# Kernel optimization log

Hardware: AMD Instinct MI355X
Metric: run time of the kernel (lower is better)

The kernel has to match this reference:

```python
import jax, jax.numpy as jnp
import numpy as np

B, T, F, G, H, N, C = 32, 64, 32, 32, 256, 20000, 32
EPS = 1e-5


def setup_inputs() -> dict:
    key = jax.random.key(0)
    ks = jax.random.split(key, 24)
    s = 0.05
    d = {}
    d["data_feats"] = jax.random.normal(ks[0], (B, T, F), jnp.float32)
    d["gat_output"] = jax.random.normal(ks[1], (B, N, G), jnp.float32)
    d["row_ids"] = jax.random.randint(ks[2], (B, T), 0, 2 * N, jnp.int32)
    d["node_ids"] = jax.random.randint(ks[3], (N,), 0, 2 * N, jnp.int32)
    # shared LSTM (2 layers): layer0 input F+G, layer1 input H; b = b_ih + b_hh fused
    d["shared_Wih0"] = jax.random.normal(ks[4], (4 * H, F + G)) * s
    d["shared_Whh0"] = jax.random.normal(ks[5], (4 * H, H)) * s
    d["shared_b0"] = jax.random.normal(ks[6], (4 * H,)) * s
    d["shared_Wih1"] = jax.random.normal(ks[7], (4 * H, H)) * s
    d["shared_Whh1"] = jax.random.normal(ks[8], (4 * H, H)) * s
    d["shared_b1"] = jax.random.normal(ks[9], (4 * H,)) * s
    # act/time/timeR LSTMs stacked on leading axis 3, each 2 layers of [4H,H]
    d["heads_Wih"] = jax.random.normal(ks[10], (3, 2, 4 * H, H)) * s
    d["heads_Whh"] = jax.random.normal(ks[11], (3, 2, 4 * H, H)) * s
    d["heads_b"] = jax.random.normal(ks[12], (3, 2, 4 * H)) * s
    d["bn_gnn_g"] = jnp.ones((G,), jnp.float32)
    d["bn_gnn_b"] = jnp.zeros((G,), jnp.float32)
    d["bn_shared_g"] = jnp.ones((H,), jnp.float32)
    d["bn_shared_b"] = jnp.zeros((H,), jnp.float32)
    d["heads_bn_g"] = jnp.ones((3, H), jnp.float32)
    d["heads_bn_b"] = jnp.zeros((3, H), jnp.float32)
    d["fc_act_W"] = jax.random.normal(ks[13], (C, H)) * s
    d["fc_act_b"] = jnp.zeros((C,), jnp.float32)
    d["fc_time_W"] = jax.random.normal(ks[14], (1, H)) * s
    d["fc_time_b"] = jnp.zeros((1,), jnp.float32)
    d["fc_timeR_W"] = jax.random.normal(ks[15], (1, H)) * s
    d["fc_timeR_b"] = jnp.zeros((1,), jnp.float32)
    return d


def batchnorm(x, gamma, beta):
    # BatchNorm1d training-mode: stats over (batch, length) per channel; x: [B, L, C]
    mean = jnp.mean(x, axis=(0, 1))
    var = jnp.var(x, axis=(0, 1))
    return (x - mean) * (gamma / jnp.sqrt(var + EPS)) + beta


def lstm_layer(x, Wih, Whh, b):
    # x: [B, T, Din]; PyTorch gate order i, f, g, o
    xp = jnp.einsum("btf,gf->btg", x, Wih) + b  # [B, T, 4H]
    h = Whh.shape[1]
    init = (jnp.zeros((x.shape[0], h), x.dtype), jnp.zeros((x.shape[0], h), x.dtype))

    def step(carry, xt):
        hprev, cprev = carry
        gates = xt + hprev @ Whh.T
        i, f, g, o = jnp.split(gates, 4, axis=-1)
        c = jax.nn.sigmoid(f) * cprev + jax.nn.sigmoid(i) * jnp.tanh(g)
        hnew = jax.nn.sigmoid(o) * jnp.tanh(c)
        return (hnew, c), hnew

    _, hs = jax.lax.scan(step, init, jnp.swapaxes(xp, 0, 1))
    return jnp.swapaxes(hs, 0, 1)  # [B, T, H]


def reference(data_feats, gat_output, row_ids, node_ids,
              shared_Wih0, shared_Whh0, shared_b0,
              shared_Wih1, shared_Whh1, shared_b1,
              heads_Wih, heads_Whh, heads_b,
              bn_gnn_g, bn_gnn_b, bn_shared_g, bn_shared_b,
              heads_bn_g, heads_bn_b,
              fc_act_W, fc_act_b, fc_time_W, fc_time_b, fc_timeR_W, fc_timeR_b):
    # --- graph branch: BN over GAT output, value-match lookup + gather ---
    gat_norm = batchnorm(gat_output, bn_gnn_g, bn_gnn_b)  # [B, N, G]
    eq = row_ids[:, :, None] == node_ids[None, None, :]   # [B, T, N]
    idx = jnp.argmax(eq, axis=-1)                          # first matching index
    found = jnp.any(eq, axis=-1)
    gathered = jnp.take_along_axis(gat_norm, idx[:, :, None], axis=1)  # [B, T, G]
    matched = jnp.where(found[:, :, None], gathered, 0.0)
    lstm_in = jnp.concatenate([data_feats, matched], axis=-1)  # [B, T, F+G]

    # --- shared 2-layer LSTM + BN (dropout off / eval) ---
    shared = lstm_layer(lstm_in, shared_Wih0, shared_Whh0, shared_b0)
    shared = lstm_layer(shared, shared_Wih1, shared_Whh1, shared_b1)
    shared = batchnorm(shared, bn_shared_g, bn_shared_b)

    # --- act / time / timeR head LSTMs (vmapped over the 3 heads) + BN ---
    def head(Wih, Whh, b, g, bb):
        hh = lstm_layer(shared, Wih[0], Whh[0], b[0])
        hh = lstm_layer(hh, Wih[1], Whh[1], b[1])
        return batchnorm(hh, g, bb)

    heads = jax.vmap(head)(heads_Wih, heads_Whh, heads_b, heads_bn_g, heads_bn_b)
    last = heads[:, :, -1, :]  # [3, B, H]

    act = jax.nn.softmax(last[0] @ fc_act_W.T + fc_act_b, axis=1)
    time = last[1] @ fc_time_W.T + fc_time_b
    timeR = last[2] @ fc_timeR_W.T + fc_timeR_b
    return act, time, timeR
```

## Files before the change

### kernel.cpp

```cpp
#include <hip/hip_runtime.h>
#include <hip/hip_fp16.h>
#include <math.h>

#define Bn 32
#define Tn 64
#define Fdim 32
#define Gdim 32
#define Hdim 256
#define Ndim 20000
#define Cdim 32
#define G4 1024
#define BT 2048
#define EPSc 1e-5f

__device__ __forceinline__ float sigmoidf_(float x){ return 1.0f/(1.0f + __expf(-x)); }
__device__ __forceinline__ float tanhf_(float x){ return 2.0f/(1.0f+__expf(-2.0f*x)) - 1.0f; }

typedef _Float16 h2t __attribute__((ext_vector_type(2)));

__device__ __forceinline__ float fdot2_(unsigned w, unsigned h, float acc){
#if defined(__has_builtin) && __has_builtin(__builtin_amdgcn_fdot2)
  return __builtin_amdgcn_fdot2(__builtin_bit_cast(h2t, w), __builtin_bit_cast(h2t, h), acc, false);
#else
  h2t a = __builtin_bit_cast(h2t, w), b = __builtin_bit_cast(h2t, h);
  acc = fmaf((float)a.x, (float)b.x, acc);
  return fmaf((float)a.y, (float)b.y, acc);
#endif
}

__device__ __forceinline__ unsigned packh_(float lo, float hi){
  unsigned ulo = (unsigned)__half_as_ushort(__float2half(lo));
  unsigned uhi = (unsigned)__half_as_ushort(__float2half(hi));
  return ulo | (uhi << 16);
}

__global__ void init_kernel(float* ws){
  int i = blockIdx.x*256 + threadIdx.x;
  if (i < 2112) ws[i] = 0.0f;
  int* table = (int*)(ws + 2112);
  if (i < 40000) table[i] = 0x7fffffff;
}

__global__ void bn_stats_kernel(const float* __restrict__ gat, float* __restrict__ sums){
  __shared__ float ss[256], sq[256];
  int tid = threadIdx.x;
  int idx = blockIdx.x*256 + tid;
  int stride = gridDim.x*256;
  const int total = Bn*Ndim*Gdim;
  float s=0.f,q=0.f;
  for (int i=idx; i<total; i+=stride){ float v = gat[i]; s+=v; q+=v*v; }
  ss[tid]=s; sq[tid]=q; __syncthreads();
  for (int off=128; off>=32; off>>=1){
    if(tid<off){ ss[tid]+=ss[tid+off]; sq[tid]+=sq[tid+off]; }
    __syncthreads();
  }
  if (tid<32){ atomicAdd(&sums[tid], ss[tid]); atomicAdd(&sums[32+tid], sq[tid]); }
}

__global__ void table_kernel(const int* __restrict__ node_ids, int* __restrict__ table){
  int i = blockIdx.x*256 + threadIdx.x;
  if (i < Ndim) atomicMin(&table[node_ids[i]], i);
}

__global__ void build_input_kernel(const float* __restrict__ feats, const float* __restrict__ gat,
    const int* __restrict__ row_ids, const int* __restrict__ table, const float* __restrict__ sums,
    const float* __restrict__ bng, const float* __restrict__ bnb, unsigned* __restrict__ out){
  int gt = blockIdx.x*256 + threadIdx.x;
  int pos = gt >> 5; int k2 = gt & 31;
  float lo, hi;
  if (k2 < 16){
    float2 v = *(const float2*)(feats + pos*Fdim + 2*k2);
    lo = v.x; hi = v.y;
  } else {
    int g0 = 2*(k2-16);
    int r = row_ids[pos];
    int idx = table[r];
    if (idx < Ndim){
      int b = pos / Tn;
      float2 x = *(const float2*)(gat + (size_t)(b*Ndim + idx)*Gdim + g0);
      const float cnt = (float)(Bn*Ndim);
      float m0 = sums[g0]/cnt,   v0 = sums[32+g0]/cnt - m0*m0;
      float m1 = sums[g0+1]/cnt, v1 = sums[32+g0+1]/cnt - m1*m1;
      lo = (x.x-m0)*bng[g0]*rsqrtf(v0+EPSc) + bnb[g0];
      hi = (x.y-m1)*bng[g0+1]*rsqrtf(v1+EPSc) + bnb[g0+1];
    } else { lo = 0.0f; hi = 0.0f; }
  }
  out[gt] = packh_(lo, hi);
}

struct TArgs { const float* src[8]; unsigned* dst[8]; int K[8]; };
__global__ void packwih_kernel(TArgs a){
  __shared__ unsigned tile[32][33];
  int mat = blockIdx.y;
  int K = a.K[mat];
  int K2 = K >> 1;
  int ktiles = K2 >> 5;
  int tk = blockIdx.x & 3;
  int tn = blockIdx.x >> 2;
  if (tk >= ktiles) return;
  const float* src = a.src[mat];
  unsigned* dst = a.dst[mat];
  int tx = threadIdx.x, ty = threadIdx.y;
  int n0 = tn*32, k2_0 = tk*32;
  #pragma unroll
  for (int i=0;i<4;i++){
    int nn = ty + 8*i;
    const float* p = src + (size_t)(n0+nn)*K + 2*(k2_0 + tx);
    tile[nn][tx] = packh_(p[0], p[1]);
  }
  __syncthreads();
  #pragma unroll
  for (int i=0;i<4;i++){
    int r = ty + 8*i;
    dst[(size_t)(k2_0 + r)*G4 + n0 + tx] = tile[tx][r];
  }
}

struct PkArgs { const float* src[8]; };
__global__ void pack_kernel(PkArgs a, unsigned* __restrict__ dst){
  int gid = blockIdx.x*256 + threadIdx.x;
  int m = gid >> 17;
  int rem = gid & 0x1FFFF;
  int q = rem & 3;
  int t2 = (rem >> 2) & 1023;
  int ci = rem >> 12;
  int c = ci >> 3, i = ci & 7;
  int j = t2 & 255, kq = t2 >> 8;
  int r = 4*j + c;
  int k = kq*64 + 8*i + 2*q;
  const float* W = a.src[m];
  dst[gid] = packh_(W[r*256 + k], W[r*256 + k + 1]);
}

struct PArgs { const unsigned* x[3]; const unsigned* wt[3]; const float* bias[3]; float* out[3]; int K2; };
__global__ __launch_bounds__(256) void proj_kernel(PArgs a){
  int hd = blockIdx.z;
  int n  = blockIdx.y*256 + threadIdx.x;
  int m0 = blockIdx.x*8;
  int K2 = a.K2;
  const unsigned* xh = a.x[hd] + (size_t)m0*K2;
  const unsigned* wt = a.wt[hd];
  float bv = a.bias[hd][n];
  float acc[8];
  #pragma unroll
  for (int i=0;i<8;i++) acc[i]=bv;
  for (int k2=0;k2<K2;k2+=4){
    unsigned w0 = wt[(size_t)(k2+0)*G4+n];
    unsigned w1 = wt[(size_t)(k2+1)*G4+n];
    unsigned w2 = wt[(size_t)(k2+2)*G4+n];
    unsigned w3 = wt[(size_t)(k2+3)*G4+n];
    #pragma unroll
    for (int i=0;i<8;i++){
      uint4 xv = *(const uint4*)(xh + i*K2 + k2);
      acc[i]=fdot2_(w0,xv.x,acc[i]); acc[i]=fdot2_(w1,xv.y,acc[i]);
      acc[i]=fdot2_(w2,xv.z,acc[i]); acc[i]=fdot2_(w3,xv.w,acc[i]);
    }
  }
  float* out = a.out[hd] + (size_t)m0*G4 + n;
  #pragma unroll
  for (int i=0;i<8;i++) out[i*G4]=acc[i];
}

struct RArgs { const float* xp[3]; const unsigned* wt[3]; float* out[3]; unsigned* outh[3]; };
__global__ __launch_bounds__(1024,1) void rec_kernel(RArgs a){
  extern __shared__ float lds[];
  unsigned* lw   = (unsigned*)lds;
  float*    part = lds + 32768;
  unsigned* hp   = (unsigned*)(lds + 36864);
  int b = blockIdx.x, hd = blockIdx.y, tid = threadIdx.x;
  int j = tid & 255, kq = tid >> 8;
  const float* xp = a.xp[hd] + (size_t)b*Tn*G4;
  const unsigned* wt = a.wt[hd];
  float* out = a.out[hd] + (size_t)b*Tn*Hdim;
  unsigned* outh = a.outh[hd] + (size_t)b*Tn*128;

  unsigned w[96];
  #pragma unroll
  for (int c=0;c<4;c++){
    #pragma unroll
    for (int i=0;i<6;i++){
      uint4 v = *(const uint4*)(wt + ((c*8+i)*1024 + tid)*4);
      w[(c*6+i)*4+0]=v.x; w[(c*6+i)*4+1]=v.y; w[(c*6+i)*4+2]=v.z; w[(c*6+i)*4+3]=v.w;
    }
    #pragma unroll
    for (int i=6;i<8;i++){
      uint4 v = *(const uint4*)(wt + ((c*8+i)*1024 + tid)*4);
      *(uint4*)(lw + ((c*2+(i-6))*1024 + tid)*4) = v;
    }
  }
  float cst = 0.0f;
  if (tid < 128){ hp[tid] = 0u; hp[128+tid] = 0u; }
  __syncthreads();

  int p = 0;
  for (int t=0; t<Tn; t++){
    float ac0, ac1, ac2, ac3;
    if (kq == 0){
      float4 xv = *(const float4*)(xp + t*G4 + 4*j);
      ac0=xv.x; ac1=xv.y; ac2=xv.z; ac3=xv.w;
    } else { ac0=0.f; ac1=0.f; ac2=0.f; ac3=0.f; }
    const unsigned* hrow = hp + p*128 + kq*32;
    #pragma unroll
    for (int ic=0; ic<6; ic++){
      uint4 hv = *(const uint4*)(hrow + 4*ic);
      ac0=fdot2_(w[0*24+ic*4+0],hv.x,ac0); ac0=fdot2_(w[0*24+ic*4+1],hv.y,ac0);
      ac0=fdot2_(w[0*24+ic*4+2],hv.z,ac0); ac0=fdot2_(w[0*24+ic*4+3],hv.w,ac0);
      ac1=fdot2_(w[1*24+ic*4+0],hv.x,ac1); ac1=fdot2_(w[1*24+ic*4+1],hv.y,ac1);
      ac1=fdot2_(w[1*24+ic*4+2],hv.z,ac1); ac1=fdot2_(w[1*24+ic*4+3],hv.w,ac1);
      ac2=fdot2_(w[2*24+ic*4+0],hv.x,ac2); ac2=fdot2_(w[2*24+ic*4+1],hv.y,ac2);
      ac2=fdot2_(w[2*24+ic*4+2],hv.z,ac2); ac2=fdot2_(w[2*24+ic*4+3],hv.w,ac2);
      ac3=fdot2_(w[3*24+ic*4+0],hv.x,ac3); ac3=fdot2_(w[3*24+ic*4+1],hv.y,ac3);
      ac3=fdot2_(w[3*24+ic*4+2],hv.z,ac3); ac3=fdot2_(w[3*24+ic*4+3],hv.w,ac3);
    }
    #pragma unroll
    for (int ic=6; ic<8; ic++){
      uint4 hv = *(const uint4*)(hrow + 4*ic);
      { uint4 lv = *(const uint4*)(lw + ((0*2+(ic-6))*1024 + tid)*4);
        ac0=fdot2_(lv.x,hv.x,ac0); ac0=fdot2_(lv.y,hv.y,ac0);
        ac0=fdot2_(lv.z,hv.z,ac0); ac0=fdot2_(lv.w,hv.w,ac0); }
      { uint4 lv = *(const uint4*)(lw + ((1*2+(ic-6))*1024 + tid)*4);
        ac1=fdot2_(lv.x,hv.x,ac1); ac1=fdot2_(lv.y,hv.y,ac1);
        ac1=fdot2_(lv.z,hv.z,ac1); ac1=fdot2_(lv.w,hv.w,ac1); }
      { uint4 lv = *(const uint4*)(lw + ((2*2+(ic-6))*1024 + tid)*4);
        ac2=fdot2_(lv.x,hv.x,ac2); ac2=fdot2_(lv.y,hv.y,ac2);
        ac2=fdot2_(lv.z,hv.z,ac2); ac2=fdot2_(lv.w,hv.w,ac2); }
      { uint4 lv = *(const uint4*)(lw + ((3*2+(ic-6))*1024 + tid)*4);
        ac3=fdot2_(lv.x,hv.x,ac3); ac3=fdot2_(lv.y,hv.y,ac3);
        ac3=fdot2_(lv.z,hv.z,ac3); ac3=fdot2_(lv.w,hv.w,ac3); }
    }
    *(float4*)(part + kq*1024 + 4*j) = make_float4(ac0,ac1,ac2,ac3);
    __syncthreads();
    if (tid < 256){
      int u = tid;
      float gi = part[u]     + part[1024+u]     + part[2048+u]     + part[3072+u];
      float gf = part[256+u] + part[1024+256+u] + part[2048+256+u] + part[3072+256+u];
      float gg = part[512+u] + part[1024+512+u] + part[2048+512+u] + part[3072+512+u];
      float go = part[768+u] + part[1024+768+u] + part[2048+768+u] + part[3072+768+u];
      cst = sigmoidf_(gf)*cst + sigmoidf_(gi)*tanhf_(gg);
      float h = sigmoidf_(go)*tanhf_(cst);
      out[t*Hdim + u] = h;
      float hpartner = __shfl_xor(h, 1);
      if ((u & 1) == 0){
        unsigned hh = packh_(h, hpartner);
        hp[(p^1)*128 + (u>>1)] = hh;
        outh[t*128 + (u>>1)] = hh;
      }
    }
    __syncthreads();
    p ^= 1;
  }
}

struct SArgs { const float* in[3]; float* stats[3]; };
__global__ void stats_kernel(SArgs a){
  int hd = blockIdx.y; int tid = threadIdx.x;
  const float* in = a.in[hd] + blockIdx.x*256*Hdim;
  float s=0.f,q=0.f;
  for (int r=0;r<256;r++){ float v = in[r*Hdim + tid]; s+=v; q+=v*v; }
  atomicAdd(&a.stats[hd][tid], s);
  atomicAdd(&a.stats[hd][Hdim+tid], q);
}

__global__ void norm_kernel(const float* __restrict__ in, const float* __restrict__ stats,
   const float* __restrict__ g, const float* __restrict__ bta, unsigned* __restrict__ outh){
  int i2 = blockIdx.x*256 + threadIdx.x;
  int h2 = i2 & 127; int m = i2 >> 7;
  int h0 = 2*h2;
  float2 v = *(const float2*)(in + (size_t)m*Hdim + h0);
  float m0 = stats[h0]*(1.0f/BT),   v0 = stats[Hdim+h0]*(1.0f/BT) - m0*m0;
  float m1 = stats[h0+1]*(1.0f/BT), v1 = stats[Hdim+h0+1]*(1.0f/BT) - m1*m1;
  float lo = (v.x-m0)*g[h0]*rsqrtf(v0+EPSc) + bta[h0];
  float hi = (v.y-m1)*g[h0+1]*rsqrtf(v1+EPSc) + bta[h0+1];
  outh[i2] = packh_(lo, hi);
}

__global__ __launch_bounds__(256) void final_kernel(
  const float* __restrict__ h0, const float* __restrict__ h1, const float* __restrict__ h2,
  const float* __restrict__ stats,
  const float* __restrict__ hbg, const float* __restrict__ hbb,
  const float* __restrict__ actW, const float* __restrict__ actB,
  const float* __restrict__ tW, const float* __restrict__ tB,
  const float* __restrict__ rW, const float* __restrict__ rB,
  float* __restrict__ outp){
  __shared__ float v0[Bn*Hdim];
  __shared__ float lg[Bn*Cdim];
  int tid = threadIdx.x;
  for (int i=tid; i<Bn*Hdim; i+=256){
    int b=i>>8, h=i&255;
    float sm = stats[512 + h], sq = stats[512+256+h];
    float mean = sm*(1.0f/BT); float var = sq*(1.0f/BT) - mean*mean;
    v0[i] = (h0[(b*Tn+63)*Hdim + h] - mean)*hbg[h]*rsqrtf(var+EPSc) + hbb[h];
  }
  __syncthreads();
  for (int i=tid; i<Bn*Cdim; i+=256){
    int b=i>>5, cc=i&31;
    float acc = actB[cc];
    const float* wrow = actW + cc*Hdim;
    const float* vrow = v0 + b*Hdim;
    #pragma unroll 4
    for (int h=0;h<Hdim;h++) acc = fmaf(vrow[h], wrow[h], acc);
    lg[i] = acc;
  }
  __syncthreads();
  if (tid < Bn){
    int b = tid;
    float m = -1e30f;
    #pragma unroll
    for (int cc=0; cc<Cdim; cc++) m = fmaxf(m, lg[b*Cdim+cc]);
    float e[Cdim]; float s = 0.f;
    #pragma unroll
    for (int cc=0; cc<Cdim; cc++){ float ee = __expf(lg[b*Cdim+cc]-m); e[cc]=ee; s+=ee; }
    float inv = 1.0f/s;
    #pragma unroll
    for (int cc=0; cc<Cdim; cc++) outp[b*Cdim+cc] = e[cc]*inv;
  }
  if (tid < 64){
    int b = tid & 31; int w = tid >> 5;
    const float* hh = w ? h2 : h1;
    const float* fw = w ? rW : tW;
    float fb = w ? rB[0] : tB[0];
    int hd = 1 + w;
    float acc = fb;
    for (int h=0; h<Hdim; h++){
      float sm = stats[(1+hd)*512 + h], sq = stats[(1+hd)*512+256+h];
      float mean = sm*(1.0f/BT); float var = sq*(1.0f/BT) - mean*mean;
      float v = (hh[(b*Tn+63)*Hdim + h] - mean)*hbg[hd*Hdim+h]*rsqrtf(var+EPSc) + hbb[hd*Hdim+h];
      acc = fmaf(v, fw[h], acc);
    }
    outp[1024 + w*32 + b] = acc;
  }
}

extern "C" void kernel_launch(void* const* d_in, const int* in_sizes, int n_in,
                              void* d_out, int out_size, void* d_ws, size_t ws_size,
                              hipStream_t stream){
  const float* data_feats = (const float*)d_in[0];
  const float* gat   = (const float*)d_in[1];
  const int*   row_ids  = (const int*)d_in[2];
  const int*   node_ids = (const int*)d_in[3];
  const float* sWih0 = (const float*)d_in[4];
  const float* sWhh0 = (const float*)d_in[5];
  const float* sb0   = (const float*)d_in[6];
  const float* sWih1 = (const float*)d_in[7];
  const float* sWhh1 = (const float*)d_in[8];
  const float* sb1   = (const float*)d_in[9];
  const float* hWih  = (const float*)d_in[10];
  const float* hWhh  = (const float*)d_in[11];
  const float* hb    = (const float*)d_in[12];
  const float* bng   = (const float*)d_in[13];
  const float* bnb   = (const float*)d_in[14];
  const float* bsg   = (const float*)d_in[15];
  const float* bsb   = (const float*)d_in[16];
  const float* hbg   = (const float*)d_in[17];
  const float* hbb   = (const float*)d_in[18];
  const float* actW  = (const float*)d_in[19];
  const float* actB  = (const float*)d_in[20];
  const float* tW    = (const float*)d_in[21];
  const float* tB    = (const float*)d_in[22];
  const float* rW    = (const float*)d_in[23];
  const float* rB    = (const float*)d_in[24];
  float* ws  = (float*)d_ws;
  float* out = (float*)d_out;

  const size_t S_GAT = 0;
  const size_t S_BN  = 64;
  const size_t TABLE = 2112;
  const size_t WIHP  = 42112;
  const size_t PSLOT = 131072;
  const size_t WHHP  = WIHP + 8*PSLOT;
  const size_t LSTM_INH = WHHP + 8*PSLOT;
  const size_t XPOFF = LSTM_INH + 65536;
  const size_t BUF0H = XPOFF + 3*2097152;
  const size_t BUF1  = BUF0H + 262144;
  const size_t BUFNH = BUF1 + 524288;
  const size_t HB0H  = BUFNH + 262144;
  const size_t HB1   = HB0H + 3*262144;

  const int REC_LDS = 148480;
  hipFuncSetAttribute((const void*)rec_kernel, hipFuncAttributeMaxDynamicSharedMemorySize, REC_LDS);

  init_kernel<<<157,256,0,stream>>>(ws);
  bn_stats_kernel<<<2048,256,0,stream>>>(gat, ws+S_GAT);
  table_kernel<<<(Ndim+255)/256,256,0,stream>>>(node_ids, (int*)(ws+TABLE));
  build_input_kernel<<<256,256,0,stream>>>(data_feats, gat, row_ids, (int*)(ws+TABLE),
                                           ws+S_GAT, bng, bnb, (unsigned*)(ws+LSTM_INH));

  unsigned* wih = (unsigned*)(ws + WIHP);
  TArgs ta;
  ta.src[0]=sWih0; ta.K[0]=64;
  ta.src[1]=sWih1; ta.K[1]=256;
  for (int hd=0; hd<3; hd++) for (int l=0;l<2;l++){
    ta.src[2+hd*2+l] = hWih + (size_t)(hd*2+l)*G4*Hdim; ta.K[2+hd*2+l] = 256;
  }
  for (int i=0;i<8;i++) ta.dst[i] = wih + (size_t)i*PSLOT;
  packwih_kernel<<<dim3(128,8),dim3(32,8),0,stream>>>(ta);

  unsigned* whh = (unsigned*)(ws + WHHP);
  PkArgs pka;
  pka.src[0]=sWhh0; pka.src[1]=sWhh1;
  for (int hd=0; hd<3; hd++) for (int l=0;l<2;l++)
    pka.src[2+hd*2+l] = hWhh + (size_t)(hd*2+l)*G4*Hdim;
  pack_kernel<<<4096,256,0,stream>>>(pka, whh);

  PArgs pa; RArgs ra; SArgs sa;
  pa.K2=32; pa.x[0]=(unsigned*)(ws+LSTM_INH); pa.wt[0]=wih+0*PSLOT; pa.bias[0]=sb0; pa.out[0]=ws+XPOFF;
  proj_kernel<<<dim3(256,4,1),256,0,stream>>>(pa);
  ra.xp[0]=ws+XPOFF; ra.wt[0]=whh+0*PSLOT; ra.out[0]=ws+BUF1;  ra.outh[0]=(unsigned*)(ws+BUF0H);
  rec_kernel<<<dim3(32,1),1024,REC_LDS,stream>>>(ra);
  pa.K2=128; pa.x[0]=(unsigned*)(ws+BUF0H); pa.wt[0]=wih+1*PSLOT; pa.bias[0]=sb1; pa.out[0]=ws+XPOFF;
  proj_kernel<<<dim3(256,4,1),256,0,stream>>>(pa);
  ra.xp[0]=ws+XPOFF; ra.wt[0]=whh+1*PSLOT; ra.out[0]=ws+BUF1; ra.outh[0]=(unsigned*)(ws+BUF0H);
  rec_kernel<<<dim3(32,1),1024,REC_LDS,stream>>>(ra);
  sa.in[0]=ws+BUF1; sa.stats[0]=ws+S_BN;
  stats_kernel<<<dim3(8,1),256,0,stream>>>(sa);
  norm_kernel<<<1024,256,0,stream>>>(ws+BUF1, ws+S_BN, bsg, bsb, (unsigned*)(ws+BUFNH));
  pa.K2=128;
  for (int hd=0;hd<3;hd++){
    pa.x[hd]=(unsigned*)(ws+BUFNH); pa.wt[hd]=wih+(size_t)(2+hd*2)*PSLOT; pa.bias[hd]=hb + (size_t)(hd*2)*G4;
    pa.out[hd]=ws+XPOFF+(size_t)hd*2097152;
  }
  proj_kernel<<<dim3(256,4,3),256,0,stream>>>(pa);
  for (int hd=0;hd<3;hd++){
    ra.xp[hd]=ws+XPOFF+(size_t)hd*2097152; ra.wt[hd]=whh+(size_t)(2+hd*2)*PSLOT;
    ra.out[hd]=ws+HB1+(size_t)hd*524288;  ra.outh[hd]=(unsigned*)(ws+HB0H)+(size_t)hd*262144;
  }
  rec_kernel<<<dim3(32,3),1024,REC_LDS,stream>>>(ra);
  for (int hd=0;hd<3;hd++){
    pa.x[hd]=(unsigned*)(ws+HB0H)+(size_t)hd*262144; pa.wt[hd]=wih+(size_t)(2+hd*2+1)*PSLOT;
    pa.bias[hd]=hb + (size_t)(hd*2+1)*G4;
    pa.out[hd]=ws+XPOFF+(size_t)hd*2097152;
  }
  proj_kernel<<<dim3(256,4,3),256,0,stream>>>(pa);
  for (int hd=0;hd<3;hd++){
    ra.xp[hd]=ws+XPOFF+(size_t)hd*2097152; ra.wt[hd]=whh+(size_t)(2+hd*2+1)*PSLOT;
    ra.out[hd]=ws+HB1+(size_t)hd*524288; ra.outh[hd]=(unsigned*)(ws+HB0H)+(size_t)hd*262144;
  }
  rec_kernel<<<dim3(32,3),1024,REC_LDS,stream>>>(ra);
  for (int hd=0;hd<3;hd++){ sa.in[hd]=ws+HB1+(size_t)hd*524288; sa.stats[hd]=ws+S_BN+(size_t)(1+hd)*512; }
  stats_kernel<<<dim3(8,3),256,0,stream>>>(sa);
  final_kernel<<<1,256,0,stream>>>(ws+HB1, ws+HB1+524288, ws+HB1+2*524288, ws+S_BN,
                                   hbg, hbb, actW, actB, tW, tB, rW, rB, out);
}
```

Measured before the change: 865.2 us.

## Fuse all LSTM pipeline stages into one cooperative persistent kernel

Replaces the sequence of roughly fifteen separate launches (init, GAT stats, lookup table, input build, weight packing, projections, recurrences, BN stats/normalisation, final head) with a single cooperative kernel of 256 blocks of 1024 threads. Stages are separated by grid-wide syncs, so the inter-kernel launch gaps and tail effects go away. In exchange, the recurrent phases leave most blocks idle at the grid barrier. The Wih packing loses its LDS-tiled transpose and now reads strided. Every stage is also forced to run at one block per CU with the large recurrent LDS allocation.

```diff
diff --git a/kernel.cpp b/kernel.cpp
--- a/kernel.cpp
+++ b/kernel.cpp
@@ -1,6 +1,9 @@
 #include <hip/hip_runtime.h>
 #include <hip/hip_fp16.h>
+#include <hip/hip_cooperative_groups.h>
 #include <math.h>
+
+namespace cg = cooperative_groups;
 
 #define Bn 32
 #define Tn 64
@@ -13,6 +16,22 @@
 #define BT 2048
 #define EPSc 1e-5f
 
+#define S_GAT   0u
+#define S_BN    64u
+#define TABLE   2112u
+#define WIHP    42112u
+#define PSLOT   131072u
+#define WHHP    (WIHP + 8*PSLOT)
+#define LSTM_INH (WHHP + 8*PSLOT)
+#define XPOFF   (LSTM_INH + 65536)
+#define BUF0H   (XPOFF + 3*2097152)
+#define BUF1    (BUF0H + 262144)
+#define BUFNH   (BUF1 + 524288)
+#define HB0H    (BUFNH + 262144)
+#define HB1     (HB0H + 3*262144)
+
+#define GTHREADS 262144
+
 __device__ __forceinline__ float sigmoidf_(float x){ return 1.0f/(1.0f + __expf(-x)); }
 __device__ __forceinline__ float tanhf_(float x){ return 2.0f/(1.0f+__expf(-2.0f*x)) - 1.0f; }
 
@@ -34,113 +53,14 @@
   return ulo | (uhi << 16);
 }
 
-__global__ void init_kernel(float* ws){
-  int i = blockIdx.x*256 + threadIdx.x;
-  if (i < 2112) ws[i] = 0.0f;
-  int* table = (int*)(ws + 2112);
-  if (i < 40000) table[i] = 0x7fffffff;
-}
-
-__global__ void bn_stats_kernel(const float* __restrict__ gat, float* __restrict__ sums){
-  __shared__ float ss[256], sq[256];
-  int tid = threadIdx.x;
-  int idx = blockIdx.x*256 + tid;
-  int stride = gridDim.x*256;
-  const int total = Bn*Ndim*Gdim;
-  float s=0.f,q=0.f;
-  for (int i=idx; i<total; i+=stride){ float v = gat[i]; s+=v; q+=v*v; }
-  ss[tid]=s; sq[tid]=q; __syncthreads();
-  for (int off=128; off>=32; off>>=1){
-    if(tid<off){ ss[tid]+=ss[tid+off]; sq[tid]+=sq[tid+off]; }
-    __syncthreads();
-  }
-  if (tid<32){ atomicAdd(&sums[tid], ss[tid]); atomicAdd(&sums[32+tid], sq[tid]); }
-}
-
-__global__ void table_kernel(const int* __restrict__ node_ids, int* __restrict__ table){
-  int i = blockIdx.x*256 + threadIdx.x;
-  if (i < Ndim) atomicMin(&table[node_ids[i]], i);
-}
-
-__global__ void build_input_kernel(const float* __restrict__ feats, const float* __restrict__ gat,
-    const int* __restrict__ row_ids, const int* __restrict__ table, const float* __restrict__ sums,
-    const float* __restrict__ bng, const float* __restrict__ bnb, unsigned* __restrict__ out){
-  int gt = blockIdx.x*256 + threadIdx.x;
-  int pos = gt >> 5; int k2 = gt & 31;
-  float lo, hi;
-  if (k2 < 16){
-    float2 v = *(const float2*)(feats + pos*Fdim + 2*k2);
-    lo = v.x; hi = v.y;
-  } else {
-    int g0 = 2*(k2-16);
-    int r = row_ids[pos];
-    int idx = table[r];
-    if (idx < Ndim){
-      int b = pos / Tn;
-      float2 x = *(const float2*)(gat + (size_t)(b*Ndim + idx)*Gdim + g0);
-      const float cnt = (float)(Bn*Ndim);
-      float m0 = sums[g0]/cnt,   v0 = sums[32+g0]/cnt - m0*m0;
-      float m1 = sums[g0+1]/cnt, v1 = sums[32+g0+1]/cnt - m1*m1;
-      lo = (x.x-m0)*bng[g0]*rsqrtf(v0+EPSc) + bnb[g0];
-      hi = (x.y-m1)*bng[g0+1]*rsqrtf(v1+EPSc) + bnb[g0+1];
-    } else { lo = 0.0f; hi = 0.0f; }
-  }
-  out[gt] = packh_(lo, hi);
-}
-
-struct TArgs { const float* src[8]; unsigned* dst[8]; int K[8]; };
-__global__ void packwih_kernel(TArgs a){
-  __shared__ unsigned tile[32][33];
-  int mat = blockIdx.y;
-  int K = a.K[mat];
-  int K2 = K >> 1;
-  int ktiles = K2 >> 5;
-  int tk = blockIdx.x & 3;
-  int tn = blockIdx.x >> 2;
-  if (tk >= ktiles) return;
-  const float* src = a.src[mat];
-  unsigned* dst = a.dst[mat];
-  int tx = threadIdx.x, ty = threadIdx.y;
-  int n0 = tn*32, k2_0 = tk*32;
-  #pragma unroll
-  for (int i=0;i<4;i++){
-    int nn = ty + 8*i;
-    const float* p = src + (size_t)(n0+nn)*K + 2*(k2_0 + tx);
-    tile[nn][tx] = packh_(p[0], p[1]);
-  }
-  __syncthreads();
-  #pragma unroll
-  for (int i=0;i<4;i++){
-    int r = ty + 8*i;
-    dst[(size_t)(k2_0 + r)*G4 + n0 + tx] = tile[tx][r];
-  }
-}
-
-struct PkArgs { const float* src[8]; };
-__global__ void pack_kernel(PkArgs a, unsigned* __restrict__ dst){
-  int gid = blockIdx.x*256 + threadIdx.x;
-  int m = gid >> 17;
-  int rem = gid & 0x1FFFF;
-  int q = rem & 3;
-  int t2 = (rem >> 2) & 1023;
-  int ci = rem >> 12;
-  int c = ci >> 3, i = ci & 7;
-  int j = t2 & 255, kq = t2 >> 8;
-  int r = 4*j + c;
-  int k = kq*64 + 8*i + 2*q;
-  const float* W = a.src[m];
-  dst[gid] = packh_(W[r*256 + k], W[r*256 + k + 1]);
-}
-
-struct PArgs { const unsigned* x[3]; const unsigned* wt[3]; const float* bias[3]; float* out[3]; int K2; };
-__global__ __launch_bounds__(256) void proj_kernel(PArgs a){
-  int hd = blockIdx.z;
-  int n  = blockIdx.y*256 + threadIdx.x;
-  int m0 = blockIdx.x*8;
-  int K2 = a.K2;
-  const unsigned* xh = a.x[hd] + (size_t)m0*K2;
-  const unsigned* wt = a.wt[hd];
-  float bv = a.bias[hd][n];
+__device__ __forceinline__ void proj_dev(const unsigned* __restrict__ x,
+    const unsigned* __restrict__ wt, const float* __restrict__ bias,
+    float* __restrict__ outp, int K2, int v, int lane){
+  int mtile = v & 255, nblk = v >> 8;
+  int n = nblk*256 + lane;
+  int m0 = mtile*8;
+  const unsigned* xh = x + (size_t)m0*K2;
+  float bv = bias[n];
   float acc[8];
   #pragma unroll
   for (int i=0;i<8;i++) acc[i]=bv;
@@ -156,23 +76,18 @@
       acc[i]=fdot2_(w2,xv.z,acc[i]); acc[i]=fdot2_(w3,xv.w,acc[i]);
     }
   }
-  float* out = a.out[hd] + (size_t)m0*G4 + n;
+  float* op = outp + (size_t)m0*G4 + n;
   #pragma unroll
-  for (int i=0;i<8;i++) out[i*G4]=acc[i];
-}
-
-struct RArgs { const float* xp[3]; const unsigned* wt[3]; float* out[3]; unsigned* outh[3]; };
-__global__ __launch_bounds__(1024,1) void rec_kernel(RArgs a){
-  extern __shared__ float lds[];
+  for (int i=0;i<8;i++) op[i*G4]=acc[i];
+}
+
+__device__ __forceinline__ void rec_dev(float* lds, const float* __restrict__ xp,
+    const unsigned* __restrict__ wt, float* __restrict__ out,
+    unsigned* __restrict__ outh, int tid){
   unsigned* lw   = (unsigned*)lds;
   float*    part = lds + 32768;
   unsigned* hp   = (unsigned*)(lds + 36864);
-  int b = blockIdx.x, hd = blockIdx.y, tid = threadIdx.x;
   int j = tid & 255, kq = tid >> 8;
-  const float* xp = a.xp[hd] + (size_t)b*Tn*G4;
-  const unsigned* wt = a.wt[hd];
-  float* out = a.out[hd] + (size_t)b*Tn*Hdim;
-  unsigned* outh = a.outh[hd] + (size_t)b*Tn*128;
 
   unsigned w[96];
   #pragma unroll
@@ -251,193 +166,276 @@
   }
 }
 
-struct SArgs { const float* in[3]; float* stats[3]; };
-__global__ void stats_kernel(SArgs a){
-  int hd = blockIdx.y; int tid = threadIdx.x;
-  const float* in = a.in[hd] + blockIdx.x*256*Hdim;
-  float s=0.f,q=0.f;
-  for (int r=0;r<256;r++){ float v = in[r*Hdim + tid]; s+=v; q+=v*v; }
-  atomicAdd(&a.stats[hd][tid], s);
-  atomicAdd(&a.stats[hd][Hdim+tid], q);
-}
-
-__global__ void norm_kernel(const float* __restrict__ in, const float* __restrict__ stats,
-   const float* __restrict__ g, const float* __restrict__ bta, unsigned* __restrict__ outh){
-  int i2 = blockIdx.x*256 + threadIdx.x;
-  int h2 = i2 & 127; int m = i2 >> 7;
-  int h0 = 2*h2;
-  float2 v = *(const float2*)(in + (size_t)m*Hdim + h0);
-  float m0 = stats[h0]*(1.0f/BT),   v0 = stats[Hdim+h0]*(1.0f/BT) - m0*m0;
-  float m1 = stats[h0+1]*(1.0f/BT), v1 = stats[Hdim+h0+1]*(1.0f/BT) - m1*m1;
-  float lo = (v.x-m0)*g[h0]*rsqrtf(v0+EPSc) + bta[h0];
-  float hi = (v.y-m1)*g[h0+1]*rsqrtf(v1+EPSc) + bta[h0+1];
-  outh[i2] = packh_(lo, hi);
-}
-
-__global__ __launch_bounds__(256) void final_kernel(
-  const float* __restrict__ h0, const float* __restrict__ h1, const float* __restrict__ h2,
-  const float* __restrict__ stats,
-  const float* __restrict__ hbg, const float* __restrict__ hbb,
-  const float* __restrict__ actW, const float* __restrict__ actB,
-  const float* __restrict__ tW, const float* __restrict__ tB,
-  const float* __restrict__ rW, const float* __restrict__ rB,
-  float* __restrict__ outp){
-  __shared__ float v0[Bn*Hdim];
-  __shared__ float lg[Bn*Cdim];
-  int tid = threadIdx.x;
-  for (int i=tid; i<Bn*Hdim; i+=256){
-    int b=i>>8, h=i&255;
-    float sm = stats[512 + h], sq = stats[512+256+h];
-    float mean = sm*(1.0f/BT); float var = sq*(1.0f/BT) - mean*mean;
-    v0[i] = (h0[(b*Tn+63)*Hdim + h] - mean)*hbg[h]*rsqrtf(var+EPSc) + hbb[h];
-  }
-  __syncthreads();
-  for (int i=tid; i<Bn*Cdim; i+=256){
-    int b=i>>5, cc=i&31;
-    float acc = actB[cc];
-    const float* wrow = actW + cc*Hdim;
-    const float* vrow = v0 + b*Hdim;
-    #pragma unroll 4
-    for (int h=0;h<Hdim;h++) acc = fmaf(vrow[h], wrow[h], acc);
-    lg[i] = acc;
-  }
-  __syncthreads();
-  if (tid < Bn){
-    int b = tid;
-    float m = -1e30f;
-    #pragma unroll
-    for (int cc=0; cc<Cdim; cc++) m = fmaxf(m, lg[b*Cdim+cc]);
-    float e[Cdim]; float s = 0.f;
-    #pragma unroll
-    for (int cc=0; cc<Cdim; cc++){ float ee = __expf(lg[b*Cdim+cc]-m); e[cc]=ee; s+=ee; }
-    float inv = 1.0f/s;
-    #pragma unroll
-    for (int cc=0; cc<Cdim; cc++) outp[b*Cdim+cc] = e[cc]*inv;
-  }
-  if (tid < 64){
-    int b = tid & 31; int w = tid >> 5;
-    const float* hh = w ? h2 : h1;
-    const float* fw = w ? rW : tW;
-    float fb = w ? rB[0] : tB[0];
-    int hd = 1 + w;
-    float acc = fb;
-    for (int h=0; h<Hdim; h++){
-      float sm = stats[(1+hd)*512 + h], sq = stats[(1+hd)*512+256+h];
+struct MegaArgs {
+  const float *feats, *gat;
+  const int *row_ids, *node_ids;
+  const float *sWih0, *sWhh0, *sb0, *sWih1, *sWhh1, *sb1;
+  const float *hWih, *hWhh, *hb;
+  const float *bng, *bnb, *bsg, *bsb, *hbg, *hbb;
+  const float *actW, *actB, *tW, *tB, *rW, *rB;
+  float* ws; float* out;
+};
+
+__global__ __launch_bounds__(1024,1) void mega_kernel(MegaArgs a){
+  extern __shared__ float lds[];
+  cg::grid_group grd = cg::this_grid();
+  const int tid = threadIdx.x;
+  const int bid = blockIdx.x;
+  const int gid = bid*1024 + tid;
+  float* ws = a.ws;
+  int* table = (int*)(ws + TABLE);
+  unsigned* wih = (unsigned*)(ws + WIHP);
+  unsigned* whh = (unsigned*)(ws + WHHP);
+
+  if (gid < 2112) ws[gid] = 0.0f;
+  for (int i = gid; i < 40000; i += GTHREADS) table[i] = 0x7fffffff;
+  grd.sync();
+
+  if (gid < Ndim) atomicMin(&table[a.node_ids[gid]], gid);
+  {
+    float* ss = lds; float* sq = lds + 1024;
+    const int total = Bn*Ndim*Gdim;
+    float s=0.f,q=0.f;
+    for (int i = gid; i < total; i += GTHREADS){ float v = a.gat[i]; s+=v; q+=v*v; }
+    ss[tid]=s; sq[tid]=q; __syncthreads();
+    for (int off=512; off>=32; off>>=1){
+      if (tid<off){ ss[tid]+=ss[tid+off]; sq[tid]+=sq[tid+off]; }
+      __syncthreads();
+    }
+    if (tid<32){ atomicAdd(&ws[S_GAT+tid], ss[tid]); atomicAdd(&ws[S_GAT+32+tid], sq[tid]); }
+  }
+  grd.sync();
+
+  {
+    const float* sums = ws + S_GAT;
+    unsigned* outp = (unsigned*)(ws + LSTM_INH);
+    for (int gt = gid; gt < BT*32; gt += GTHREADS){
+      int pos = gt >> 5; int k2 = gt & 31;
+      float lo, hi;
+      if (k2 < 16){
+        float2 v = *(const float2*)(a.feats + pos*Fdim + 2*k2);
+        lo = v.x; hi = v.y;
+      } else {
+        int g0 = 2*(k2-16);
+        int r = a.row_ids[pos];
+        int idx = table[r];
+        if (idx < Ndim){
+          int b = pos / Tn;
+          float2 x = *(const float2*)(a.gat + (size_t)(b*Ndim + idx)*Gdim + g0);
+          const float cnt = (float)(Bn*Ndim);
+          float m0 = sums[g0]/cnt,   v0 = sums[32+g0]/cnt - m0*m0;
+          float m1 = sums[g0+1]/cnt, v1 = sums[32+g0+1]/cnt - m1*m1;
+          lo = (x.x-m0)*a.bng[g0]*rsqrtf(v0+EPSc) + a.bnb[g0];
+          hi = (x.y-m1)*a.bng[g0+1]*rsqrtf(v1+EPSc) + a.bnb[g0+1];
+        } else { lo = 0.0f; hi = 0.0f; }
+      }
+      outp[gt] = packh_(lo, hi);
+    }
+    for (int f = gid; f < 950272; f += GTHREADS){
+      int mat, idx;
+      if (f < 32768){ mat = 0; idx = f; }
+      else { int r = f - 32768; mat = 1 + (r >> 17); idx = r & 131071; }
+      int K = (mat==0) ? 64 : 256;
+      int k2 = idx >> 10, n = idx & 1023;
+      const float* src = (mat==0) ? a.sWih0 : (mat==1) ? a.sWih1
+                         : a.hWih + (size_t)(mat-2)*G4*Hdim;
+      const float* p = src + (size_t)n*K + 2*k2;
+      wih[(size_t)mat*PSLOT + (size_t)k2*G4 + n] = packh_(p[0], p[1]);
+    }
+    for (int g2 = gid; g2 < 1048576; g2 += GTHREADS){
+      int m = g2 >> 17;
+      int rem = g2 & 0x1FFFF;
+      int q = rem & 3;
+      int t2 = (rem >> 2) & 1023;
+      int ci = rem >> 12;
+      int c = ci >> 3, i = ci & 7;
+      int j = t2 & 255, kq = t2 >> 8;
+      int r = 4*j + c;
+      int k = kq*64 + 8*i + 2*q;
+      const float* W = (m==0) ? a.sWhh0 : (m==1) ? a.sWhh1
+                       : a.hWhh + (size_t)(m-2)*G4*Hdim;
+      whh[g2] = packh_(W[r*256 + k], W[r*256 + k + 1]);
+    }
+  }
+  grd.sync();
+
+  { int v = bid*4 + (tid>>8), lane = tid & 255;
+    proj_dev((const unsigned*)(ws+LSTM_INH), wih, a.sb0, ws+XPOFF, 32, v, lane); }
+  grd.sync();
+
+  if (bid < 32)
+    rec_dev(lds, ws+XPOFF + (size_t)bid*Tn*G4, whh,
+            ws+BUF1 + (size_t)bid*Tn*Hdim,
+            (unsigned*)(ws+BUF0H) + (size_t)bid*Tn*128, tid);
+  grd.sync();
+
+  { int v = bid*4 + (tid>>8), lane = tid & 255;
+    proj_dev((const unsigned*)(ws+BUF0H), wih + PSLOT, a.sb1, ws+XPOFF, 128, v, lane); }
+  grd.sync();
+
+  if (bid < 32)
+    rec_dev(lds, ws+XPOFF + (size_t)bid*Tn*G4, whh + PSLOT,
+            ws+BUF1 + (size_t)bid*Tn*Hdim,
+            (unsigned*)(ws+BUF0H) + (size_t)bid*Tn*128, tid);
+  grd.sync();
+
+  { int vb = bid*4 + (tid>>8), lane = tid & 255;
+    if (vb < 8){
+      const float* in = ws+BUF1 + (size_t)vb*256*Hdim;
+      float s=0.f,q=0.f;
+      for (int r2=0;r2<256;r2++){ float v = in[r2*Hdim + lane]; s+=v; q+=v*v; }
+      atomicAdd(&ws[S_BN+lane], s);
+      atomicAdd(&ws[S_BN+Hdim+lane], q);
+    } }
+  grd.sync();
+
+  { const float* stats = ws + S_BN;
+    int i2 = gid;
+    int h2 = i2 & 127; int m2 = i2 >> 7;
+    int h0 = 2*h2;
+    float2 v = *(const float2*)(ws+BUF1 + (size_t)m2*Hdim + h0);
+    float m0 = stats[h0]*(1.0f/BT),   v0 = stats[Hdim+h0]*(1.0f/BT) - m0*m0;
+    float m1 = stats[h0+1]*(1.0f/BT), v1 = stats[Hdim+h0+1]*(1.0f/BT) - m1*m1;
+    float lo = (v.x-m0)*a.bsg[h0]*rsqrtf(v0+EPSc) + a.bsb[h0];
+    float hi = (v.y-m1)*a.bsg[h0+1]*rsqrtf(v1+EPSc) + a.bsb[h0+1];
+    ((unsigned*)(ws+BUFNH))[i2] = packh_(lo, hi); }
+  grd.sync();
+
+  for (int hd=0; hd<3; hd++){
+    int v = bid*4 + (tid>>8), lane = tid & 255;
+    proj_dev((const unsigned*)(ws+BUFNH), wih + (size_t)(2+hd*2)*PSLOT,
+             a.hb + (size_t)(hd*2)*G4, ws+XPOFF + (size_t)hd*2097152, 128, v, lane);
+  }
+  grd.sync();
+
+  if (bid < 96){
+    int hd = bid >> 5, b = bid & 31;
+    rec_dev(lds, ws+XPOFF + (size_t)hd*2097152 + (size_t)b*Tn*G4,
+            whh + (size_t)(2+hd*2)*PSLOT,
+            ws+HB1 + (size_t)hd*524288 + (size_t)b*Tn*Hdim,
+            (unsigned*)(ws+HB0H) + (size_t)hd*262144 + (size_t)b*Tn*128, tid);
+  }
+  grd.sync();
+
+  for (int hd=0; hd<3; hd++){
+    int v = bid*4 + (tid>>8), lane = tid & 255;
+    proj_dev((const unsigned*)(ws+HB0H) + (size_t)hd*262144,
+             wih + (size_t)(2+hd*2+1)*PSLOT,
+             a.hb + (size_t)(hd*2+1)*G4, ws+XPOFF + (size_t)hd*2097152, 128, v, lane);
+  }
+  grd.sync();
+
+  if (bid < 96){
+    int hd = bid >> 5, b = bid & 31;
+    rec_dev(lds, ws+XPOFF + (size_t)hd*2097152 + (size_t)b*Tn*G4,
+            whh + (size_t)(2+hd*2+1)*PSLOT,
+            ws+HB1 + (size_t)hd*524288 + (size_t)b*Tn*Hdim,
+            (unsigned*)(ws+HB0H) + (size_t)hd*262144 + (size_t)b*Tn*128, tid);
+  }
+  grd.sync();
+
+  { int vb = bid*4 + (tid>>8), lane = tid & 255;
+    if (vb < 24){
+      int hd = vb >> 3, blk = vb & 7;
+      const float* in = ws+HB1 + (size_t)hd*524288 + (size_t)blk*256*Hdim;
+      float* st = ws + S_BN + (size_t)(1+hd)*512;
+      float s=0.f,q=0.f;
+      for (int r2=0;r2<256;r2++){ float v = in[r2*Hdim + lane]; s+=v; q+=v*v; }
+      atomicAdd(&st[lane], s);
+      atomicAdd(&st[Hdim+lane], q);
+    } }
+  grd.sync();
+
+  if (bid == 0){
+    float* v0 = lds;
+    float* lg = lds + 8192;
+    const float* stats = ws + S_BN;
+    const float* h0 = ws + HB1;
+    const float* h1 = ws + HB1 + 524288;
+    const float* h2 = ws + HB1 + 2*524288;
+    float* outp = a.out;
+    for (int i=tid; i<Bn*Hdim; i+=1024){
+      int b=i>>8, h=i&255;
+      float sm = stats[512 + h], sq = stats[512+256+h];
       float mean = sm*(1.0f/BT); float var = sq*(1.0f/BT) - mean*mean;
-      float v = (hh[(b*Tn+63)*Hdim + h] - mean)*hbg[hd*Hdim+h]*rsqrtf(var+EPSc) + hbb[hd*Hdim+h];
-      acc = fmaf(v, fw[h], acc);
-    }
-    outp[1024 + w*32 + b] = acc;
+      v0[i] = (h0[(b*Tn+63)*Hdim + h] - mean)*a.hbg[h]*rsqrtf(var+EPSc) + a.hbb[h];
+    }
+    __syncthreads();
+    { int i = tid;
+      int b=i>>5, cc=i&31;
+      float acc = a.actB[cc];
+      const float* wrow = a.actW + cc*Hdim;
+      const float* vrow = v0 + b*Hdim;
+      #pragma unroll 4
+      for (int h=0;h<Hdim;h++) acc = fmaf(vrow[h], wrow[h], acc);
+      lg[i] = acc; }
+    __syncthreads();
+    if (tid < Bn){
+      int b = tid;
+      float m = -1e30f;
+      #pragma unroll
+      for (int cc=0; cc<Cdim; cc++) m = fmaxf(m, lg[b*Cdim+cc]);
+      float e[Cdim]; float s = 0.f;
+      #pragma unroll
+      for (int cc=0; cc<Cdim; cc++){ float ee = __expf(lg[b*Cdim+cc]-m); e[cc]=ee; s+=ee; }
+      float inv = 1.0f/s;
+      #pragma unroll
+      for (int cc=0; cc<Cdim; cc++) outp[b*Cdim+cc] = e[cc]*inv;
+    }
+    if (tid < 64){
+      int b = tid & 31; int w = tid >> 5;
+      const float* hh = w ? h2 : h1;
+      const float* fw = w ? a.rW : a.tW;
+      float fb = w ? a.rB[0] : a.tB[0];
+      int hd = 1 + w;
+      float acc = fb;
+      for (int h=0; h<Hdim; h++){
+        float sm = stats[(1+hd)*512 + h], sq = stats[(1+hd)*512+256+h];
+        float mean = sm*(1.0f/BT); float var = sq*(1.0f/BT) - mean*mean;
+        float v = (hh[(b*Tn+63)*Hdim + h] - mean)*a.hbg[hd*Hdim+h]*rsqrtf(var+EPSc) + a.hbb[hd*Hdim+h];
+        acc = fmaf(v, fw[h], acc);
+      }
+      outp[1024 + w*32 + b] = acc;
+    }
   }
 }
 
 extern "C" void kernel_launch(void* const* d_in, const int* in_sizes, int n_in,
                               void* d_out, int out_size, void* d_ws, size_t ws_size,
                               hipStream_t stream){
-  const float* data_feats = (const float*)d_in[0];
-  const float* gat   = (const float*)d_in[1];
-  const int*   row_ids  = (const int*)d_in[2];
-  const int*   node_ids = (const int*)d_in[3];
-  const float* sWih0 = (const float*)d_in[4];
-  const float* sWhh0 = (const float*)d_in[5];
-  const float* sb0   = (const float*)d_in[6];
-  const float* sWih1 = (const float*)d_in[7];
-  const float* sWhh1 = (const float*)d_in[8];
-  const float* sb1   = (const float*)d_in[9];
-  const float* hWih  = (const float*)d_in[10];
-  const float* hWhh  = (const float*)d_in[11];
-  const float* hb    = (const float*)d_in[12];
-  const float* bng   = (const float*)d_in[13];
-  const float* bnb   = (const float*)d_in[14];
-  const float* bsg   = (const float*)d_in[15];
-  const float* bsb   = (const float*)d_in[16];
-  const float* hbg   = (const float*)d_in[17];
-  const float* hbb   = (const float*)d_in[18];
-  const float* actW  = (const float*)d_in[19];
-  const float* actB  = (const float*)d_in[20];
-  const float* tW    = (const float*)d_in[21];
-  const float* tB    = (const float*)d_in[22];
-  const float* rW    = (const float*)d_in[23];
-  const float* rB    = (const float*)d_in[24];
-  float* ws  = (float*)d_ws;
-  float* out = (float*)d_out;
-
-  const size_t S_GAT = 0;
-  const size_t S_BN  = 64;
-  const size_t TABLE = 2112;
-  const size_t WIHP  = 42112;
-  const size_t PSLOT = 131072;
-  const size_t WHHP  = WIHP + 8*PSLOT;
-  const size_t LSTM_INH = WHHP + 8*PSLOT;
-  const size_t XPOFF = LSTM_INH + 65536;
-  const size_t BUF0H = XPOFF + 3*2097152;
-  const size_t BUF1  = BUF0H + 262144;
-  const size_t BUFNH = BUF1 + 524288;
-  const size_t HB0H  = BUFNH + 262144;
-  const size_t HB1   = HB0H + 3*262144;
+  MegaArgs ma;
+  ma.feats   = (const float*)d_in[0];
+  ma.gat     = (const float*)d_in[1];
+  ma.row_ids = (const int*)d_in[2];
+  ma.node_ids= (const int*)d_in[3];
+  ma.sWih0   = (const float*)d_in[4];
+  ma.sWhh0   = (const float*)d_in[5];
+  ma.sb0     = (const float*)d_in[6];
+  ma.sWih1   = (const float*)d_in[7];
+  ma.sWhh1   = (const float*)d_in[8];
+  ma.sb1     = (const float*)d_in[9];
+  ma.hWih    = (const float*)d_in[10];
+  ma.hWhh    = (const float*)d_in[11];
+  ma.hb      = (const float*)d_in[12];
+  ma.bng     = (const float*)d_in[13];
+  ma.bnb     = (const float*)d_in[14];
+  ma.bsg     = (const float*)d_in[15];
+  ma.bsb     = (const float*)d_in[16];
+  ma.hbg     = (const float*)d_in[17];
+  ma.hbb     = (const float*)d_in[18];
+  ma.actW    = (const float*)d_in[19];
+  ma.actB    = (const float*)d_in[20];
+  ma.tW      = (const float*)d_in[21];
+  ma.tB      = (const float*)d_in[22];
+  ma.rW      = (const float*)d_in[23];
+  ma.rB      = (const float*)d_in[24];
+  ma.ws      = (float*)d_ws;
+  ma.out     = (float*)d_out;
 
   const int REC_LDS = 148480;
-  hipFuncSetAttribute((const void*)rec_kernel, hipFuncAttributeMaxDynamicSharedMemorySize, REC_LDS);
-
-  init_kernel<<<157,256,0,stream>>>(ws);
-  bn_stats_kernel<<<2048,256,0,stream>>>(gat, ws+S_GAT);
-  table_kernel<<<(Ndim+255)/256,256,0,stream>>>(node_ids, (int*)(ws+TABLE));
-  build_input_kernel<<<256,256,0,stream>>>(data_feats, gat, row_ids, (int*)(ws+TABLE),
-                                           ws+S_GAT, bng, bnb, (unsigned*)(ws+LSTM_INH));
-
-  unsigned* wih = (unsigned*)(ws + WIHP);
-  TArgs ta;
-  ta.src[0]=sWih0; ta.K[0]=64;
-  ta.src[1]=sWih1; ta.K[1]=256;
-  for (int hd=0; hd<3; hd++) for (int l=0;l<2;l++){
-    ta.src[2+hd*2+l] = hWih + (size_t)(hd*2+l)*G4*Hdim; ta.K[2+hd*2+l] = 256;
-  }
-  for (int i=0;i<8;i++) ta.dst[i] = wih + (size_t)i*PSLOT;
-  packwih_kernel<<<dim3(128,8),dim3(32,8),0,stream>>>(ta);
-
-  unsigned* whh = (unsigned*)(ws + WHHP);
-  PkArgs pka;
-  pka.src[0]=sWhh0; pka.src[1]=sWhh1;
-  for (int hd=0; hd<3; hd++) for (int l=0;l<2;l++)
-    pka.src[2+hd*2+l] = hWhh + (size_t)(hd*2+l)*G4*Hdim;
-  pack_kernel<<<4096,256,0,stream>>>(pka, whh);
-
-  PArgs pa; RArgs ra; SArgs sa;
-  pa.K2=32; pa.x[0]=(unsigned*)(ws+LSTM_INH); pa.wt[0]=wih+0*PSLOT; pa.bias[0]=sb0; pa.out[0]=ws+XPOFF;
-  proj_kernel<<<dim3(256,4,1),256,0,stream>>>(pa);
-  ra.xp[0]=ws+XPOFF; ra.wt[0]=whh+0*PSLOT; ra.out[0]=ws+BUF1;  ra.outh[0]=(unsigned*)(ws+BUF0H);
-  rec_kernel<<<dim3(32,1),1024,REC_LDS,stream>>>(ra);
-  pa.K2=128; pa.x[0]=(unsigned*)(ws+BUF0H); pa.wt[0]=wih+1*PSLOT; pa.bias[0]=sb1; pa.out[0]=ws+XPOFF;
-  proj_kernel<<<dim3(256,4,1),256,0,stream>>>(pa);
-  ra.xp[0]=ws+XPOFF; ra.wt[0]=whh+1*PSLOT; ra.out[0]=ws+BUF1; ra.outh[0]=(unsigned*)(ws+BUF0H);
-  rec_kernel<<<dim3(32,1),1024,REC_LDS,stream>>>(ra);
-  sa.in[0]=ws+BUF1; sa.stats[0]=ws+S_BN;
-  stats_kernel<<<dim3(8,1),256,0,stream>>>(sa);
-  norm_kernel<<<1024,256,0,stream>>>(ws+BUF1, ws+S_BN, bsg, bsb, (unsigned*)(ws+BUFNH));
-  pa.K2=128;
-  for (int hd=0;hd<3;hd++){
-    pa.x[hd]=(unsigned*)(ws+BUFNH); pa.wt[hd]=wih+(size_t)(2+hd*2)*PSLOT; pa.bias[hd]=hb + (size_t)(hd*2)*G4;
-    pa.out[hd]=ws+XPOFF+(size_t)hd*2097152;
-  }
-  proj_kernel<<<dim3(256,4,3),256,0,stream>>>(pa);
-  for (int hd=0;hd<3;hd++){
-    ra.xp[hd]=ws+XPOFF+(size_t)hd*2097152; ra.wt[hd]=whh+(size_t)(2+hd*2)*PSLOT;
-    ra.out[hd]=ws+HB1+(size_t)hd*524288;  ra.outh[hd]=(unsigned*)(ws+HB0H)+(size_t)hd*262144;
-  }
-  rec_kernel<<<dim3(32,3),1024,REC_LDS,stream>>>(ra);
-  for (int hd=0;hd<3;hd++){
-    pa.x[hd]=(unsigned*)(ws+HB0H)+(size_t)hd*262144; pa.wt[hd]=wih+(size_t)(2+hd*2+1)*PSLOT;
-    pa.bias[hd]=hb + (size_t)(hd*2+1)*G4;
-    pa.out[hd]=ws+XPOFF+(size_t)hd*2097152;
-  }
-  proj_kernel<<<dim3(256,4,3),256,0,stream>>>(pa);
-  for (int hd=0;hd<3;hd++){
-    ra.xp[hd]=ws+XPOFF+(size_t)hd*2097152; ra.wt[hd]=whh+(size_t)(2+hd*2+1)*PSLOT;
-    ra.out[hd]=ws+HB1+(size_t)hd*524288; ra.outh[hd]=(unsigned*)(ws+HB0H)+(size_t)hd*262144;
-  }
-  rec_kernel<<<dim3(32,3),1024,REC_LDS,stream>>>(ra);
-  for (int hd=0;hd<3;hd++){ sa.in[hd]=ws+HB1+(size_t)hd*524288; sa.stats[hd]=ws+S_BN+(size_t)(1+hd)*512; }
-  stats_kernel<<<dim3(8,3),256,0,stream>>>(sa);
-  final_kernel<<<1,256,0,stream>>>(ws+HB1, ws+HB1+524288, ws+HB1+2*524288, ws+S_BN,
-                                   hbg, hbb, actW, actB, tW, tB, rW, rB, out);
-}
+  hipFuncSetAttribute((const void*)mega_kernel, hipFuncAttributeMaxDynamicSharedMemorySize, REC_LDS);
+
+  void* params[] = { (void*)&ma };
+  hipLaunchCooperativeKernel((const void*)mega_kernel, dim3(256), dim3(1024),
+                             params, REC_LDS, stream);
+}
```

Result: slower. 1.491 ms (+72.3%).
